# Optimization experiments

Hardware: AMD Instinct MI355X
Metric: run time of the kernel (lower is better)

## Reference

```python
import jax, jax.numpy as jnp
import numpy as np

N_NODES = 100000
N_EDGES = 1600000
NODE_F = 64
EDGE_F = 16
OUT_F = 64


def setup_inputs() -> dict:
    key = jax.random.key(0)
    k1, k2, k3, k4, k5 = jax.random.split(key, 5)
    feat = jax.random.normal(k1, (N_NODES, NODE_F), dtype=jnp.float32)
    edge_feats = jax.random.normal(k2, (N_EDGES, EDGE_F), dtype=jnp.float32)
    src = jax.random.randint(k3, (N_EDGES,), 0, N_NODES, dtype=jnp.int64)
    dst = jax.random.randint(k4, (N_EDGES,), 0, N_NODES, dtype=jnp.int64)
    # xavier-normal-ish weight, zero bias (matches reset_parameters)
    fan_in, fan_out = NODE_F + EDGE_F, OUT_F
    std = (2.0 / (fan_in + fan_out)) ** 0.5
    weight = jax.random.normal(k5, (fan_in, fan_out), dtype=jnp.float32) * std
    bias = jnp.zeros((OUT_F,), dtype=jnp.float32)
    return {"feat": feat, "edge_feats": edge_feats, "src": src, "dst": dst,
            "weight": weight, "bias": bias}


def reference(feat, edge_feats, src, dst, weight, bias):
    N = feat.shape[0]
    # in-degree based symmetric-ish norm: pow(clamp(in_deg,1), -0.5)
    deg = jax.ops.segment_sum(jnp.ones(dst.shape, dtype=feat.dtype), dst,
                              num_segments=N)
    norm = jnp.clip(deg, 1.0) ** -0.5  # [N]
    norm = norm[:, None]
    # sum over incoming edges of concat([edge_feats, h_src]).
    # sum of concat == concat of sums, so aggregate each part separately
    # (avoids materializing the per-edge concat).
    sum_e = jax.ops.segment_sum(edge_feats, dst, num_segments=N)  # [N, E_F]
    sum_h = jax.ops.segment_sum(feat[src], dst, num_segments=N)   # [N, NODE_F]
    sum_f = jnp.concatenate([sum_e, sum_h], axis=-1)              # [N, E_F+NODE_F]
    out = (sum_f * norm) @ weight
    out = out * norm + bias
    return jax.nn.selu(out)
```

## Files before the change

kernel.cpp:

```cpp
#include <hip/hip_runtime.h>
#include <math.h>

#define N_NODES 100000
#define N_EDGES 1600000
#define OUT_F   64
#define SCAN_B  1024
#define NBLK    ((N_NODES + SCAN_B - 1) / SCAN_B)

typedef __attribute__((ext_vector_type(8))) short bf16x8;
typedef __attribute__((ext_vector_type(4))) float f32x4;

__device__ __forceinline__ unsigned short f2bf_rne(float f) {
    unsigned u = __float_as_uint(f);
    return (unsigned short)((u + 0x7fffu + ((u >> 16) & 1u)) >> 16);
}
__device__ __forceinline__ float bf2f(unsigned short h) {
    return __uint_as_float((unsigned)h << 16);
}

__global__ __launch_bounds__(256) void prep(
    const float* __restrict__ feat, const float* __restrict__ weight,
    unsigned short* __restrict__ G, unsigned* __restrict__ deg_i)
{
    int tid = threadIdx.x;
    for (int i = blockIdx.x * 256 + tid; i < N_NODES; i += gridDim.x * 256)
        deg_i[i] = 0u;

    int wv = tid >> 6, ln = tid & 63;
    int li = ln & 15, lk = ln >> 4;

    bf16x8 Whi[4][2], Wlo[4][2];
    #pragma unroll
    for (int it = 0; it < 4; ++it)
        #pragma unroll
        for (int kb = 0; kb < 2; ++kb)
            #pragma unroll
            for (int j = 0; j < 8; ++j) {
                float w = weight[(16 + kb * 32 + lk * 8 + j) * 64 + it * 16 + li];
                unsigned short h = f2bf_rne(w);
                Whi[it][kb][j] = (short)h;
                Wlo[it][kb][j] = (short)f2bf_rne(w - bf2f(h));
            }

    const int tiles = N_NODES / 16;
    for (int tile = blockIdx.x * 4 + wv; tile < tiles; tile += gridDim.x * 4) {
        int n = tile * 16 + li;
        const float* fr = feat + (size_t)n * 64 + lk * 8;

        bf16x8 Bhi[2], Blo[2];
        #pragma unroll
        for (int kb = 0; kb < 2; ++kb) {
            float4 v0 = *(const float4*)(fr + kb * 32);
            float4 v1 = *(const float4*)(fr + kb * 32 + 4);
            float vv[8] = {v0.x, v0.y, v0.z, v0.w, v1.x, v1.y, v1.z, v1.w};
            #pragma unroll
            for (int j = 0; j < 8; ++j) {
                unsigned short h = f2bf_rne(vv[j]);
                Bhi[kb][j] = (short)h;
                Blo[kb][j] = (short)f2bf_rne(vv[j] - bf2f(h));
            }
        }

        f32x4 acc[4] = {{0.f,0.f,0.f,0.f},{0.f,0.f,0.f,0.f},
                        {0.f,0.f,0.f,0.f},{0.f,0.f,0.f,0.f}};
        #pragma unroll
        for (int kb = 0; kb < 2; ++kb)
            #pragma unroll
            for (int it = 0; it < 4; ++it) {
                acc[it] = __builtin_amdgcn_mfma_f32_16x16x32_bf16(Whi[it][kb], Bhi[kb], acc[it], 0, 0, 0);
                acc[it] = __builtin_amdgcn_mfma_f32_16x16x32_bf16(Wlo[it][kb], Bhi[kb], acc[it], 0, 0, 0);
                acc[it] = __builtin_amdgcn_mfma_f32_16x16x32_bf16(Whi[it][kb], Blo[kb], acc[it], 0, 0, 0);
            }

        #pragma unroll
        for (int it = 0; it < 4; ++it) {
            ushort4 o;
            o.x = f2bf_rne(acc[it][0]);
            o.y = f2bf_rne(acc[it][1]);
            o.z = f2bf_rne(acc[it][2]);
            o.w = f2bf_rne(acc[it][3]);
            *(ushort4*)(G + (size_t)n * 64 + it * 16 + lk * 4) = o;
        }
    }
}

__global__ __launch_bounds__(256) void hist_pos(
    const int* __restrict__ dst, unsigned* __restrict__ deg_i,
    unsigned short* __restrict__ pos)
{
    int q = blockIdx.x * 256 + threadIdx.x;
    if (q >= N_EDGES / 4) return;
    int4 d = ((const int4*)dst)[q];
    ushort4 p;
    p.x = (unsigned short)atomicAdd(&deg_i[d.x], 1u);
    p.y = (unsigned short)atomicAdd(&deg_i[d.y], 1u);
    p.z = (unsigned short)atomicAdd(&deg_i[d.z], 1u);
    p.w = (unsigned short)atomicAdd(&deg_i[d.w], 1u);
    ((ushort4*)pos)[q] = p;
}

__global__ __launch_bounds__(SCAN_B) void scanA(
    const unsigned* __restrict__ deg_i, unsigned* __restrict__ bsum)
{
    __shared__ unsigned ws[16];
    int i = blockIdx.x * SCAN_B + threadIdx.x;
    unsigned v = (i < N_NODES) ? deg_i[i] : 0u;
    #pragma unroll
    for (int o = 32; o; o >>= 1) v += __shfl_down(v, o);
    if ((threadIdx.x & 63) == 0) ws[threadIdx.x >> 6] = v;
    __syncthreads();
    if (threadIdx.x < 16) {
        unsigned t = ws[threadIdx.x];
        #pragma unroll
        for (int o = 8; o; o >>= 1) t += __shfl_down(t, o);
        if (threadIdx.x == 0) bsum[blockIdx.x] = t;
    }
}

__global__ __launch_bounds__(SCAN_B) void scanC(
    const unsigned* __restrict__ deg_i, const unsigned* __restrict__ bsum,
    unsigned* __restrict__ off)
{
    __shared__ unsigned ws[17];
    int t = threadIdx.x;

    if (t < 64) {
        unsigned a = 0u;
        for (int j = t; j < (int)blockIdx.x; j += 64) a += bsum[j];
        #pragma unroll
        for (int o = 32; o; o >>= 1) a += __shfl_down(a, o);
        if (t == 0) ws[16] = a;
    }

    int i = blockIdx.x * SCAN_B + t;
    unsigned v = (i < N_NODES) ? deg_i[i] : 0u;
    unsigned x = v;
    #pragma unroll
    for (int o = 1; o < 64; o <<= 1) {
        unsigned u = __shfl_up(x, o);
        if ((t & 63) >= o) x += u;
    }
    if ((t & 63) == 63) ws[t >> 6] = x;
    __syncthreads();
    if (t < 16) {
        unsigned y = ws[t];
        #pragma unroll
        for (int o = 1; o < 16; o <<= 1) {
            unsigned u = __shfl_up(y, o);
            if (t >= o) y += u;
        }
        ws[t] = y;
    }
    __syncthreads();
    unsigned base = ws[16] + ((t >> 6) ? ws[(t >> 6) - 1] : 0u);
    unsigned excl = base + x - v;
    if (i < N_NODES) off[i] = excl;
    if (i == N_NODES - 1) off[N_NODES] = excl + v;
}

__global__ __launch_bounds__(256) void fill_kernel(
    const int* __restrict__ src, const int* __restrict__ dst,
    const unsigned short* __restrict__ pos, const unsigned* __restrict__ off,
    unsigned long long* __restrict__ csr_pack)
{
    int q = blockIdx.x * 256 + threadIdx.x;
    if (q >= N_EDGES / 4) return;
    int4 s = ((const int4*)src)[q];
    int4 d = ((const int4*)dst)[q];
    ushort4 p = ((const ushort4*)pos)[q];
    unsigned e = (unsigned)q * 4u;
    csr_pack[off[d.x] + (unsigned)p.x] =
        (unsigned long long)(unsigned)s.x | ((unsigned long long)(e + 0u) << 32);
    csr_pack[off[d.y] + (unsigned)p.y] =
        (unsigned long long)(unsigned)s.y | ((unsigned long long)(e + 1u) << 32);
    csr_pack[off[d.z] + (unsigned)p.z] =
        (unsigned long long)(unsigned)s.z | ((unsigned long long)(e + 2u) << 32);
    csr_pack[off[d.w] + (unsigned)p.w] =
        (unsigned long long)(unsigned)s.w | ((unsigned long long)(e + 3u) << 32);
}

__global__ __launch_bounds__(256) void gather_out(
    const unsigned short* __restrict__ G,
    const float* __restrict__ edge_feats,
    const unsigned long long* __restrict__ csr_pack,
    const unsigned* __restrict__ off,
    const float* __restrict__ weight,
    const float* __restrict__ bias,
    float* __restrict__ out)
{
    int tid = threadIdx.x;
    int wv = tid >> 6, ln = tid & 63;

    float We[16];
    #pragma unroll
    for (int k = 0; k < 16; ++k) We[k] = weight[k * 64 + ln];
    float b = bias[ln];

    const float SC = 1.0507009873554805f;
    const float AL = 1.6732632423543772f;

    int n = blockIdx.x * 4 + wv;
    if (n >= N_NODES) return;

    unsigned start = off[n], end = off[n + 1];
    float norm2 = 1.0f / fmaxf((float)(end - start), 1.0f);

    const int gq = ln >> 4;
    const int eq = ln >> 2;

    float gh4[4] = {0.f, 0.f, 0.f, 0.f};
    float ae4[4] = {0.f, 0.f, 0.f, 0.f};

    const ushort4* __restrict__ Gv = (const ushort4*)G;

    for (unsigned base = start; base < end; base += 64u) {
        unsigned m = min(64u, end - base);
        unsigned lo = 0u, hi = 0u;
        if ((unsigned)ln < m) {
            unsigned long long pk = csr_pack[base + (unsigned)ln];
            lo = (unsigned)pk;
            hi = (unsigned)(pk >> 32);
        }

        for (unsigned i = 0; i < m; i += 8u) {
            unsigned i0 = i + (unsigned)gq, i1 = i0 + 4u;
            unsigned s0 = __shfl(lo, (int)min(i0, m - 1u));
            unsigned s1 = __shfl(lo, (int)min(i1, m - 1u));
            ushort4 q0 = {0,0,0,0}, q1 = {0,0,0,0};
            if (i0 < m) q0 = Gv[(size_t)s0 * 16u + (unsigned)(ln & 15)];
            if (i1 < m) q1 = Gv[(size_t)s1 * 16u + (unsigned)(ln & 15)];
            gh4[0] += __uint_as_float((unsigned)q0.x << 16) + __uint_as_float((unsigned)q1.x << 16);
            gh4[1] += __uint_as_float((unsigned)q0.y << 16) + __uint_as_float((unsigned)q1.y << 16);
            gh4[2] += __uint_as_float((unsigned)q0.z << 16) + __uint_as_float((unsigned)q1.z << 16);
            gh4[3] += __uint_as_float((unsigned)q0.w << 16) + __uint_as_float((unsigned)q1.w << 16);
        }

        for (unsigned i = 0; i < m; i += 16u) {
            unsigned ie = i + (unsigned)eq;
            unsigned e0 = __shfl(hi, (int)min(ie, m - 1u));
            if (ie < m) {
                float4 v = *(const float4*)(edge_feats + (size_t)e0 * 16u + (unsigned)(ln & 3) * 4u);
                ae4[0] += v.x; ae4[1] += v.y; ae4[2] += v.z; ae4[3] += v.w;
            }
        }
    }

    #pragma unroll
    for (int c = 0; c < 4; ++c) {
        gh4[c] += __shfl_xor(gh4[c], 16);
        gh4[c] += __shfl_xor(gh4[c], 32);
        ae4[c] += __shfl_xor(ae4[c], 4);
        ae4[c] += __shfl_xor(ae4[c], 8);
        ae4[c] += __shfl_xor(ae4[c], 16);
        ae4[c] += __shfl_xor(ae4[c], 32);
    }
    int srcl = ln >> 2;
    float r0 = __shfl(gh4[0], srcl);
    float r1 = __shfl(gh4[1], srcl);
    float r2 = __shfl(gh4[2], srcl);
    float r3 = __shfl(gh4[3], srcl);
    int c = ln & 3;
    float gh = (c & 2) ? ((c & 1) ? r3 : r2) : ((c & 1) ? r1 : r0);

    float acc = gh;
    #pragma unroll
    for (int k = 0; k < 16; ++k)
        acc = fmaf(__shfl(ae4[k & 3], k >> 2), We[k], acc);

    float o = acc * norm2 + b;
    out[(size_t)n * 64u + ln] = (o > 0.f) ? SC * o : SC * AL * expm1f(o);
}

extern "C" void kernel_launch(void* const* d_in, const int* in_sizes, int n_in,
                              void* d_out, int out_size, void* d_ws, size_t ws_size,
                              hipStream_t stream) {
    const float* feat       = (const float*)d_in[0];
    const float* edge_feats = (const float*)d_in[1];
    const int*   src        = (const int*)d_in[2];
    const int*   dst        = (const int*)d_in[3];
    const float* weight     = (const float*)d_in[4];
    const float* bias       = (const float*)d_in[5];
    float* out = (float*)d_out;

    unsigned long long* csr_pack = (unsigned long long*)d_ws;
    unsigned short* G   = (unsigned short*)(csr_pack + N_EDGES);
    unsigned short* pos = G + (size_t)N_NODES * 64;
    unsigned* deg_i = (unsigned*)(pos + N_EDGES);
    unsigned* off   = deg_i + N_NODES;
    unsigned* bsum  = off + N_NODES + 1;

    prep<<<dim3(512), dim3(256), 0, stream>>>(feat, weight, G, deg_i);
    hist_pos<<<dim3((N_EDGES / 4 + 255) / 256), dim3(256), 0, stream>>>(dst, deg_i, pos);
    scanA<<<dim3(NBLK), dim3(SCAN_B), 0, stream>>>(deg_i, bsum);
    scanC<<<dim3(NBLK), dim3(SCAN_B), 0, stream>>>(deg_i, bsum, off);
    fill_kernel<<<dim3((N_EDGES / 4 + 255) / 256), dim3(256), 0, stream>>>(
        src, dst, pos, off, csr_pack);
    gather_out<<<dim3((N_NODES + 3) / 4), dim3(256), 0, stream>>>(
        G, edge_feats, csr_pack, off, weight, bias, out);
}
```

Baseline: 356.2 us.

## Fuse histogram into GEMM prep kernel and persist gather with wider unroll

The degree-histogram pass now runs in the same launch as the bf16 feature-transform GEMM, using separate block ranges, and the zeroing of deg_i moves to a memset. The gather kernel becomes a grid-stride persistent kernel with 2048 blocks. Its inner loop issues four G row loads plus the edge-feature load in a single iteration instead of two separate loops. Nontemporal loads and stores are added for csr_pack, edge_feats and out, aiming to cut launch overhead, overlap the independent work and raise memory-level parallelism, at the cost of one extra memset and a fixed grid size.

```diff
diff --git a/kernel.cpp b/kernel.cpp
--- a/kernel.cpp
+++ b/kernel.cpp
@@ -7,6 +7,10 @@
 #define SCAN_B  1024
 #define NBLK    ((N_NODES + SCAN_B - 1) / SCAN_B)
 
+#define EQ4      (N_EDGES / 4)
+#define HIST_BLK ((EQ4 + 255) / 256)
+#define GEMM_BLK 512
+
 typedef __attribute__((ext_vector_type(8))) short bf16x8;
 typedef __attribute__((ext_vector_type(4))) float f32x4;
 
@@ -18,14 +22,28 @@
     return __uint_as_float((unsigned)h << 16);
 }
 
-__global__ __launch_bounds__(256) void prep(
+__global__ __launch_bounds__(256) void prep_hist(
     const float* __restrict__ feat, const float* __restrict__ weight,
-    unsigned short* __restrict__ G, unsigned* __restrict__ deg_i)
+    const int* __restrict__ dst,
+    unsigned short* __restrict__ G, unsigned* __restrict__ deg_i,
+    unsigned short* __restrict__ pos)
 {
     int tid = threadIdx.x;
-    for (int i = blockIdx.x * 256 + tid; i < N_NODES; i += gridDim.x * 256)
-        deg_i[i] = 0u;
-
+
+    if (blockIdx.x < HIST_BLK) {
+        int q = blockIdx.x * 256 + tid;
+        if (q >= EQ4) return;
+        int4 d = ((const int4*)dst)[q];
+        ushort4 p;
+        p.x = (unsigned short)atomicAdd(&deg_i[d.x], 1u);
+        p.y = (unsigned short)atomicAdd(&deg_i[d.y], 1u);
+        p.z = (unsigned short)atomicAdd(&deg_i[d.z], 1u);
+        p.w = (unsigned short)atomicAdd(&deg_i[d.w], 1u);
+        ((ushort4*)pos)[q] = p;
+        return;
+    }
+
+    int gb = (int)blockIdx.x - HIST_BLK;
     int wv = tid >> 6, ln = tid & 63;
     int li = ln & 15, lk = ln >> 4;
 
@@ -43,7 +61,7 @@
             }
 
     const int tiles = N_NODES / 16;
-    for (int tile = blockIdx.x * 4 + wv; tile < tiles; tile += gridDim.x * 4) {
+    for (int tile = gb * 4 + wv; tile < tiles; tile += GEMM_BLK * 4) {
         int n = tile * 16 + li;
         const float* fr = feat + (size_t)n * 64 + lk * 8;
 
@@ -84,21 +102,6 @@
     }
 }
 
-__global__ __launch_bounds__(256) void hist_pos(
-    const int* __restrict__ dst, unsigned* __restrict__ deg_i,
-    unsigned short* __restrict__ pos)
-{
-    int q = blockIdx.x * 256 + threadIdx.x;
-    if (q >= N_EDGES / 4) return;
-    int4 d = ((const int4*)dst)[q];
-    ushort4 p;
-    p.x = (unsigned short)atomicAdd(&deg_i[d.x], 1u);
-    p.y = (unsigned short)atomicAdd(&deg_i[d.y], 1u);
-    p.z = (unsigned short)atomicAdd(&deg_i[d.z], 1u);
-    p.w = (unsigned short)atomicAdd(&deg_i[d.w], 1u);
-    ((ushort4*)pos)[q] = p;
-}
-
 __global__ __launch_bounds__(SCAN_B) void scanA(
     const unsigned* __restrict__ deg_i, unsigned* __restrict__ bsum)
 {
@@ -164,7 +167,7 @@
     unsigned long long* __restrict__ csr_pack)
 {
     int q = blockIdx.x * 256 + threadIdx.x;
-    if (q >= N_EDGES / 4) return;
+    if (q >= EQ4) return;
     int4 s = ((const int4*)src)[q];
     int4 d = ((const int4*)dst)[q];
     ushort4 p = ((const ushort4*)pos)[q];
@@ -199,76 +202,87 @@
     const float SC = 1.0507009873554805f;
     const float AL = 1.6732632423543772f;
 
-    int n = blockIdx.x * 4 + wv;
-    if (n >= N_NODES) return;
-
-    unsigned start = off[n], end = off[n + 1];
-    float norm2 = 1.0f / fmaxf((float)(end - start), 1.0f);
-
     const int gq = ln >> 4;
     const int eq = ln >> 2;
-
-    float gh4[4] = {0.f, 0.f, 0.f, 0.f};
-    float ae4[4] = {0.f, 0.f, 0.f, 0.f};
-
     const ushort4* __restrict__ Gv = (const ushort4*)G;
 
-    for (unsigned base = start; base < end; base += 64u) {
-        unsigned m = min(64u, end - base);
-        unsigned lo = 0u, hi = 0u;
-        if ((unsigned)ln < m) {
-            unsigned long long pk = csr_pack[base + (unsigned)ln];
-            lo = (unsigned)pk;
-            hi = (unsigned)(pk >> 32);
-        }
-
-        for (unsigned i = 0; i < m; i += 8u) {
-            unsigned i0 = i + (unsigned)gq, i1 = i0 + 4u;
-            unsigned s0 = __shfl(lo, (int)min(i0, m - 1u));
-            unsigned s1 = __shfl(lo, (int)min(i1, m - 1u));
-            ushort4 q0 = {0,0,0,0}, q1 = {0,0,0,0};
-            if (i0 < m) q0 = Gv[(size_t)s0 * 16u + (unsigned)(ln & 15)];
-            if (i1 < m) q1 = Gv[(size_t)s1 * 16u + (unsigned)(ln & 15)];
-            gh4[0] += __uint_as_float((unsigned)q0.x << 16) + __uint_as_float((unsigned)q1.x << 16);
-            gh4[1] += __uint_as_float((unsigned)q0.y << 16) + __uint_as_float((unsigned)q1.y << 16);
-            gh4[2] += __uint_as_float((unsigned)q0.z << 16) + __uint_as_float((unsigned)q1.z << 16);
-            gh4[3] += __uint_as_float((unsigned)q0.w << 16) + __uint_as_float((unsigned)q1.w << 16);
-        }
-
-        for (unsigned i = 0; i < m; i += 16u) {
-            unsigned ie = i + (unsigned)eq;
-            unsigned e0 = __shfl(hi, (int)min(ie, m - 1u));
-            if (ie < m) {
-                float4 v = *(const float4*)(edge_feats + (size_t)e0 * 16u + (unsigned)(ln & 3) * 4u);
-                ae4[0] += v.x; ae4[1] += v.y; ae4[2] += v.z; ae4[3] += v.w;
-            }
-        }
-    }
-
-    #pragma unroll
-    for (int c = 0; c < 4; ++c) {
-        gh4[c] += __shfl_xor(gh4[c], 16);
-        gh4[c] += __shfl_xor(gh4[c], 32);
-        ae4[c] += __shfl_xor(ae4[c], 4);
-        ae4[c] += __shfl_xor(ae4[c], 8);
-        ae4[c] += __shfl_xor(ae4[c], 16);
-        ae4[c] += __shfl_xor(ae4[c], 32);
-    }
-    int srcl = ln >> 2;
-    float r0 = __shfl(gh4[0], srcl);
-    float r1 = __shfl(gh4[1], srcl);
-    float r2 = __shfl(gh4[2], srcl);
-    float r3 = __shfl(gh4[3], srcl);
-    int c = ln & 3;
-    float gh = (c & 2) ? ((c & 1) ? r3 : r2) : ((c & 1) ? r1 : r0);
-
-    float acc = gh;
-    #pragma unroll
-    for (int k = 0; k < 16; ++k)
-        acc = fmaf(__shfl(ae4[k & 3], k >> 2), We[k], acc);
-
-    float o = acc * norm2 + b;
-    out[(size_t)n * 64u + ln] = (o > 0.f) ? SC * o : SC * AL * expm1f(o);
+    for (int n = blockIdx.x * 4 + wv; n < N_NODES; n += gridDim.x * 4) {
+        unsigned start = off[n], end = off[n + 1];
+        float norm2 = 1.0f / fmaxf((float)(end - start), 1.0f);
+
+        float gh4[4] = {0.f, 0.f, 0.f, 0.f};
+        float ae4[4] = {0.f, 0.f, 0.f, 0.f};
+
+        for (unsigned base = start; base < end; base += 64u) {
+            unsigned m = min(64u, end - base);
+            unsigned lo = 0u, hi = 0u;
+            if ((unsigned)ln < m) {
+                unsigned long long pk =
+                    __builtin_nontemporal_load(&csr_pack[base + (unsigned)ln]);
+                lo = (unsigned)pk;
+                hi = (unsigned)(pk >> 32);
+            }
+
+            for (unsigned i = 0; i < m; i += 16u) {
+                unsigned i0 = i + (unsigned)gq;
+                unsigned i1 = i0 + 4u, i2 = i0 + 8u, i3 = i0 + 12u;
+                unsigned s0 = __shfl(lo, (int)min(i0, m - 1u));
+                unsigned s1 = __shfl(lo, (int)min(i1, m - 1u));
+                unsigned s2 = __shfl(lo, (int)min(i2, m - 1u));
+                unsigned s3 = __shfl(lo, (int)min(i3, m - 1u));
+                unsigned ie = i + (unsigned)eq;
+                unsigned e0 = __shfl(hi, (int)min(ie, m - 1u));
+
+                ushort4 q0 = {0,0,0,0}, q1 = {0,0,0,0},
+                        q2 = {0,0,0,0}, q3 = {0,0,0,0};
+                if (i0 < m) q0 = Gv[(size_t)s0 * 16u + (unsigned)(ln & 15)];
+                if (i1 < m) q1 = Gv[(size_t)s1 * 16u + (unsigned)(ln & 15)];
+                if (i2 < m) q2 = Gv[(size_t)s2 * 16u + (unsigned)(ln & 15)];
+                if (i3 < m) q3 = Gv[(size_t)s3 * 16u + (unsigned)(ln & 15)];
+
+                f32x4 v = {0.f, 0.f, 0.f, 0.f};
+                if (ie < m)
+                    v = __builtin_nontemporal_load(
+                        (const f32x4*)(edge_feats + (size_t)e0 * 16u + (unsigned)(ln & 3) * 4u));
+
+                gh4[0] += __uint_as_float((unsigned)q0.x << 16) + __uint_as_float((unsigned)q1.x << 16)
+                        + __uint_as_float((unsigned)q2.x << 16) + __uint_as_float((unsigned)q3.x << 16);
+                gh4[1] += __uint_as_float((unsigned)q0.y << 16) + __uint_as_float((unsigned)q1.y << 16)
+                        + __uint_as_float((unsigned)q2.y << 16) + __uint_as_float((unsigned)q3.y << 16);
+                gh4[2] += __uint_as_float((unsigned)q0.z << 16) + __uint_as_float((unsigned)q1.z << 16)
+                        + __uint_as_float((unsigned)q2.z << 16) + __uint_as_float((unsigned)q3.z << 16);
+                gh4[3] += __uint_as_float((unsigned)q0.w << 16) + __uint_as_float((unsigned)q1.w << 16)
+                        + __uint_as_float((unsigned)q2.w << 16) + __uint_as_float((unsigned)q3.w << 16);
+                ae4[0] += v[0]; ae4[1] += v[1]; ae4[2] += v[2]; ae4[3] += v[3];
+            }
+        }
+
+        #pragma unroll
+        for (int c = 0; c < 4; ++c) {
+            gh4[c] += __shfl_xor(gh4[c], 16);
+            gh4[c] += __shfl_xor(gh4[c], 32);
+            ae4[c] += __shfl_xor(ae4[c], 4);
+            ae4[c] += __shfl_xor(ae4[c], 8);
+            ae4[c] += __shfl_xor(ae4[c], 16);
+            ae4[c] += __shfl_xor(ae4[c], 32);
+        }
+        int srcl = ln >> 2;
+        float r0 = __shfl(gh4[0], srcl);
+        float r1 = __shfl(gh4[1], srcl);
+        float r2 = __shfl(gh4[2], srcl);
+        float r3 = __shfl(gh4[3], srcl);
+        int c = ln & 3;
+        float gh = (c & 2) ? ((c & 1) ? r3 : r2) : ((c & 1) ? r1 : r0);
+
+        float acc = gh;
+        #pragma unroll
+        for (int k = 0; k < 16; ++k)
+            acc = fmaf(__shfl(ae4[k & 3], k >> 2), We[k], acc);
+
+        float o = acc * norm2 + b;
+        float res = (o > 0.f) ? SC * o : SC * AL * expm1f(o);
+        __builtin_nontemporal_store(res, &out[(size_t)n * 64u + ln]);
+    }
 }
 
 extern "C" void kernel_launch(void* const* d_in, const int* in_sizes, int n_in,
@@ -289,12 +303,13 @@
     unsigned* off   = deg_i + N_NODES;
     unsigned* bsum  = off + N_NODES + 1;
 
-    prep<<<dim3(512), dim3(256), 0, stream>>>(feat, weight, G, deg_i);
-    hist_pos<<<dim3((N_EDGES / 4 + 255) / 256), dim3(256), 0, stream>>>(dst, deg_i, pos);
+    hipMemsetAsync(deg_i, 0, N_NODES * sizeof(unsigned), stream);
+    prep_hist<<<dim3(HIST_BLK + GEMM_BLK), dim3(256), 0, stream>>>(
+        feat, weight, dst, G, deg_i, pos);
     scanA<<<dim3(NBLK), dim3(SCAN_B), 0, stream>>>(deg_i, bsum);
     scanC<<<dim3(NBLK), dim3(SCAN_B), 0, stream>>>(deg_i, bsum, off);
-    fill_kernel<<<dim3((N_EDGES / 4 + 255) / 256), dim3(256), 0, stream>>>(
+    fill_kernel<<<dim3(HIST_BLK), dim3(256), 0, stream>>>(
         src, dst, pos, off, csr_pack);
-    gather_out<<<dim3((N_NODES + 3) / 4), dim3(256), 0, stream>>>(
+    gather_out<<<dim3(2048), dim3(256), 0, stream>>>(
         G, edge_feats, csr_pack, off, weight, bias, out);
 }
```

Result: slower. 392.7 us (+10.3%).
